# Optimization experiments

Hardware: AMD Instinct MI355X
Metric: run time of the kernel (lower is better)

The kernel has to match this reference:

```python
import jax, jax.numpy as jnp
import numpy as np

B, N, OBS = 512, 64, 256
H1, H2 = 4, 4
D = 128            # embed/key dim (d_k_1 = d_k_2 = 128)
O1 = D // H1       # 32, per-head value dim stage 1
O2 = D // H2       # 32, per-head value dim stage 2
IN2 = O1 * H1      # 128, input dim to stage 2
FOUT = 16          # final_output_dim


def setup_inputs() -> dict:
    key = jax.random.key(0)
    ks = jax.random.split(key, 22)
    g = lambda k, shp: (jax.random.normal(k, shp, dtype=jnp.float32) * 0.05)
    inp = {
        "states": jax.random.normal(ks[0], (B, N, OBS), dtype=jnp.float32),
        # stage 1 per-head params, stacked over heads
        "E1_w": g(ks[1], (H1, D, OBS)), "E1_b": g(ks[2], (H1, D)),
        "K1_w": g(ks[3], (H1, D, D)),   "K1_b": g(ks[4], (H1, D)),
        "Q1_w": g(ks[5], (H1, D, D)),   "Q1_b": g(ks[6], (H1, D)),
        "V1_w": g(ks[7], (H1, O1, D)),  "V1_b": g(ks[8], (H1, O1)),
        # stage 2 per-head params
        "E2_w": g(ks[9], (H2, D, IN2)), "E2_b": g(ks[10], (H2, D)),
        "K2_w": g(ks[11], (H2, D, D)),  "K2_b": g(ks[12], (H2, D)),
        "Q2_w": g(ks[13], (H2, D, D)),  "Q2_b": g(ks[14], (H2, D)),
        "V2_w": g(ks[15], (H2, O2, D)), "V2_b": g(ks[16], (H2, O2)),
        # final MLP policy head
        "F1_w": g(ks[17], (64, O2 * H2)), "F1_b": g(ks[18], (64,)),
        "F2_w": g(ks[19], (FOUT, 64)),    "F2_b": g(ks[20], (FOUT,)),
    }
    return inp


def _attn_block(x, Ew, Eb, Kw, Kb, Qw, Qb, Vw, Vb, d_k):
    # x: [B,N,I]; all head loops batched via leading head axis h
    se = jax.nn.leaky_relu(jnp.einsum('bni,hdi->hbnd', x, Ew) + Eb[:, None, None, :])  # [h,B,N,D]
    k = jnp.einsum('hbnd,hed->hbne', se, Kw) + Kb[:, None, None, :]
    q = jnp.einsum('hbnd,hed->hbne', se, Qw) + Qb[:, None, None, :]
    w = jax.nn.softmax(jnp.einsum('hbne,hbme->hbnm', q, k) / jnp.sqrt(jnp.float32(d_k)), axis=-1)  # [h,B,N,N]
    v = jax.nn.leaky_relu(jnp.einsum('hbnd,hod->hbno', se, Vw) + Vb[:, None, None, :])  # [h,B,N,O]
    att = jnp.einsum('hbnm,hbmo->hbno', w, v)
    h, b, n, o = att.shape
    return jnp.transpose(att, (1, 2, 0, 3)).reshape(b, n, h * o), w


def reference(states, E1_w, E1_b, K1_w, K1_b, Q1_w, Q1_b, V1_w, V1_b,
              E2_w, E2_b, K2_w, K2_b, Q2_w, Q2_b, V2_w, V2_b,
              F1_w, F1_b, F2_w, F2_b):
    x1, w1 = _attn_block(states, E1_w, E1_b, K1_w, K1_b, Q1_w, Q1_b, V1_w, V1_b, D)
    x2, w2 = _attn_block(x1, E2_w, E2_b, K2_w, K2_b, Q2_w, Q2_b, V2_w, V2_b, D)
    h = jax.nn.leaky_relu(jnp.einsum('bnf,of->bno', x2, F1_w) + F1_b)
    policy = jax.nn.softmax(jnp.einsum('bno,po->bnp', h, F2_w) + F2_b, axis=-1)
    return policy, w1, w2
```

## Files before the change

### kernel.cpp

```cpp
#include <hip/hip_runtime.h>

typedef __attribute__((ext_vector_type(8))) short short8;
typedef __attribute__((ext_vector_type(4))) short short4v;
typedef __attribute__((ext_vector_type(4))) float f32x4;

#define MFMA(a, b, c) __builtin_amdgcn_mfma_f32_16x16x32_bf16((a), (b), (c), 0, 0, 0)

__device__ __forceinline__ short f2bf(float f) {
    union { float f; unsigned u; } v; v.f = f;
    unsigned r = v.u + 0x7fffu + ((v.u >> 16) & 1u);
    return (short)(r >> 16);
}
__device__ __forceinline__ float bf2f(short s) {
    union { unsigned u; float f; } v; v.u = ((unsigned)(unsigned short)s) << 16; return v.f;
}

struct ConvArgs { const float* src[10]; int end[10]; };

__global__ __launch_bounds__(256) void convert_weights_kernel(ConvArgs a, short* __restrict__ dst) {
    int i4 = blockIdx.x * 256 + threadIdx.x;
    int seg = 0;
#pragma unroll
    for (int s = 0; s < 9; s++) seg += (i4 >= a.end[s]) ? 1 : 0;
    int base = (seg == 0) ? 0 : a.end[seg - 1];
    float4 v = ((const float4*)a.src[seg])[i4 - base];
    short4v o; o.x = f2bf(v.x); o.y = f2bf(v.y); o.z = f2bf(v.z); o.w = f2bf(v.w);
    *(short4v*)(dst + (size_t)i4 * 4) = o;
}

#define KQ_LD  136
#define VT_LD  72
#define W_LD   72
#define OFF_K  0
#define OFF_Q  8704
#define OFF_SE 17408
#define OFF_VT 17408
#define OFF_W  8704
#define W32_LD 68
#define SMEM_SHORTS 26112

template<int IN, bool XF32>
__global__ __launch_bounds__(256, 3) void attn_stage_kernel(
    const void* __restrict__ xin,
    const short* __restrict__ Ew, const float* __restrict__ Eb,
    const short* __restrict__ Kw, const float* __restrict__ Kb,
    const short* __restrict__ Qw, const float* __restrict__ Qb,
    const short* __restrict__ Vw, const float* __restrict__ Vb,
    float* __restrict__ w_out,
    short* __restrict__ x_out)
{
    __shared__ short sm[SMEM_SHORTS];
    const int tid  = threadIdx.x;
    const int b    = blockIdx.x & 511;
    const int h    = blockIdx.x >> 9;
    const int wv   = tid >> 6;
    const int lane = tid & 63;
    const int quad = lane >> 4;
    const int l16  = lane & 15;
    const int XLD  = IN + 8;
    constexpr int NK1 = IN / 32;

    if constexpr (XF32) {
        const float* xb = (const float*)xin + (size_t)b * 64 * IN;
#pragma unroll
        for (int r = 0; r < IN / 16; r++) {
            int f4 = tid + 256 * r;
            int row = f4 / (IN / 4), c4 = f4 % (IN / 4);
            float4 v = ((const float4*)xb)[f4];
            short4v o; o.x = f2bf(v.x); o.y = f2bf(v.y); o.z = f2bf(v.z); o.w = f2bf(v.w);
            *(short4v*)&sm[row * XLD + c4 * 4] = o;
        }
    } else {
        const short* xb = (const short*)xin + (size_t)b * 64 * IN;
#pragma unroll
        for (int r = 0; r < IN / 32; r++) {
            int f8 = tid + 256 * r;
            int row = f8 / (IN / 8), c8 = f8 % (IN / 8);
            short8 v = *(const short8*)(xb + (size_t)f8 * 8);
            *(short8*)&sm[row * XLD + c8 * 8] = v;
        }
    }

    short8 ebf[NK1 * 2];
    {
        const short* ewh = Ew + (size_t)h * 128 * IN;
#pragma unroll
        for (int k0i = 0; k0i < NK1; k0i++)
#pragma unroll
            for (int j = 0; j < 2; j++)
                ebf[k0i * 2 + j] = *(const short8*)(ewh + (size_t)(wv * 32 + j * 16 + l16) * IN + k0i * 32 + quad * 8);
    }
    __syncthreads();

    short8 kbf[8];

    {
        f32x4 acc[4][2];
#pragma unroll
        for (int j = 0; j < 2; j++) {
            float bv = Eb[h * 128 + wv * 32 + j * 16 + l16];
            f32x4 c = {bv, bv, bv, bv};
#pragma unroll
            for (int i = 0; i < 4; i++) acc[i][j] = c;
        }
#pragma unroll
        for (int k0i = 0; k0i < NK1; k0i++) {
            short8 a[4];
#pragma unroll
            for (int i = 0; i < 4; i++)
                a[i] = *(const short8*)&sm[(i * 16 + l16) * XLD + k0i * 32 + quad * 8];
#pragma unroll
            for (int i = 0; i < 4; i++)
#pragma unroll
                for (int j = 0; j < 2; j++)
                    acc[i][j] = MFMA(a[i], ebf[k0i * 2 + j], acc[i][j]);
        }
        {
            const short* kwh = Kw + (size_t)h * 128 * 128;
#pragma unroll
            for (int k0i = 0; k0i < 4; k0i++)
#pragma unroll
                for (int j = 0; j < 2; j++)
                    kbf[k0i * 2 + j] = *(const short8*)(kwh + (size_t)(wv * 32 + j * 16 + l16) * 128 + k0i * 32 + quad * 8);
        }
#pragma unroll
        for (int i = 0; i < 4; i++)
#pragma unroll
            for (int j = 0; j < 2; j++)
#pragma unroll
                for (int r = 0; r < 4; r++) {
                    float v = acc[i][j][r];
                    v = (v >= 0.f) ? v : 0.01f * v;
                    sm[OFF_SE + (i * 16 + quad * 4 + r) * KQ_LD + wv * 32 + j * 16 + l16] = f2bf(v);
                }
    }
    __syncthreads();

    f32x4 vacc[2];
    {
        short8 qbf[8];
        const short* qwh = Qw + (size_t)h * 128 * 128;
#pragma unroll
        for (int k0i = 0; k0i < 4; k0i++)
#pragma unroll
            for (int j = 0; j < 2; j++)
                qbf[k0i * 2 + j] = *(const short8*)(qwh + (size_t)(wv * 32 + j * 16 + l16) * 128 + k0i * 32 + quad * 8);
        f32x4 kacc[4][2], qacc[4][2];
#pragma unroll
        for (int j = 0; j < 2; j++) {
            float kb = Kb[h * 128 + wv * 32 + j * 16 + l16];
            float qb = Qb[h * 128 + wv * 32 + j * 16 + l16];
            f32x4 kc = {kb, kb, kb, kb}, qc = {qb, qb, qb, qb};
#pragma unroll
            for (int i = 0; i < 4; i++) { kacc[i][j] = kc; qacc[i][j] = qc; }
        }
#pragma unroll
        for (int k0i = 0; k0i < 4; k0i++) {
            short8 a[4];
#pragma unroll
            for (int i = 0; i < 4; i++)
                a[i] = *(const short8*)&sm[OFF_SE + (i * 16 + l16) * KQ_LD + k0i * 32 + quad * 8];
#pragma unroll
            for (int i = 0; i < 4; i++)
#pragma unroll
                for (int j = 0; j < 2; j++) {
                    kacc[i][j] = MFMA(a[i], kbf[k0i * 2 + j], kacc[i][j]);
                    qacc[i][j] = MFMA(a[i], qbf[k0i * 2 + j], qacc[i][j]);
                }
        }
#pragma unroll
        for (int i = 0; i < 4; i++)
#pragma unroll
            for (int j = 0; j < 2; j++)
#pragma unroll
                for (int r = 0; r < 4; r++) {
                    int row = i * 16 + quad * 4 + r, col = wv * 32 + j * 16 + l16;
                    sm[OFF_K + row * KQ_LD + col] = f2bf(kacc[i][j][r]);
                    sm[OFF_Q + row * KQ_LD + col] = f2bf(qacc[i][j][r]);
                }
        const short* vwh = Vw + (size_t)h * 32 * 128;
        const int n0v = (wv >> 1) * 16, mrow = (wv & 1) * 32;
        short8 vbf[4];
#pragma unroll
        for (int k0i = 0; k0i < 4; k0i++)
            vbf[k0i] = *(const short8*)(vwh + (size_t)(n0v + l16) * 128 + k0i * 32 + quad * 8);
        float vb = Vb[h * 32 + n0v + l16];
        vacc[0] = (f32x4){vb, vb, vb, vb}; vacc[1] = vacc[0];
#pragma unroll
        for (int k0i = 0; k0i < 4; k0i++) {
            short8 a0 = *(const short8*)&sm[OFF_SE + (mrow + l16) * KQ_LD + k0i * 32 + quad * 8];
            short8 a1 = *(const short8*)&sm[OFF_SE + (mrow + 16 + l16) * KQ_LD + k0i * 32 + quad * 8];
            vacc[0] = MFMA(a0, vbf[k0i], vacc[0]);
            vacc[1] = MFMA(a1, vbf[k0i], vacc[1]);
        }
    }
    __syncthreads();

    {
        const int n0v = (wv >> 1) * 16, mrow = (wv & 1) * 32;
#pragma unroll
        for (int i = 0; i < 2; i++)
#pragma unroll
            for (int r = 0; r < 4; r++) {
                float v = vacc[i][r];
                v = (v >= 0.f) ? v : 0.01f * v;
                sm[OFF_VT + (n0v + l16) * VT_LD + mrow + i * 16 + quad * 4 + r] = f2bf(v);
            }
    }

    f32x4 lacc[4];
#pragma unroll
    for (int jj = 0; jj < 4; jj++) lacc[jj] = (f32x4){0.f, 0.f, 0.f, 0.f};
#pragma unroll
    for (int k0 = 0; k0 < 128; k0 += 32) {
        short8 a = *(const short8*)&sm[OFF_Q + (wv * 16 + l16) * KQ_LD + k0 + quad * 8];
#pragma unroll
        for (int jj = 0; jj < 4; jj++) {
            short8 b8 = *(const short8*)&sm[OFF_K + (jj * 16 + l16) * KQ_LD + k0 + quad * 8];
            lacc[jj] = MFMA(a, b8, lacc[jj]);
        }
    }
    __syncthreads();

    {
        const float scale = 0.08838834764831845f;
        float* w32 = (float*)sm;
        float mx[4], inv[4];
#pragma unroll
        for (int r = 0; r < 4; r++) {
            float m = lacc[0][r];
#pragma unroll
            for (int jj = 1; jj < 4; jj++) m = fmaxf(m, lacc[jj][r]);
#pragma unroll
            for (int s = 1; s < 16; s <<= 1) m = fmaxf(m, __shfl_xor(m, s, 16));
            mx[r] = m;
        }
        float sum[4] = {0.f, 0.f, 0.f, 0.f};
#pragma unroll
        for (int jj = 0; jj < 4; jj++)
#pragma unroll
            for (int r = 0; r < 4; r++) {
                float e = __expf((lacc[jj][r] - mx[r]) * scale);
                lacc[jj][r] = e; sum[r] += e;
            }
#pragma unroll
        for (int r = 0; r < 4; r++) {
#pragma unroll
            for (int s = 1; s < 16; s <<= 1) sum[r] += __shfl_xor(sum[r], s, 16);
            inv[r] = 1.0f / sum[r];
        }
#pragma unroll
        for (int r = 0; r < 4; r++) {
            int row = wv * 16 + quad * 4 + r;
#pragma unroll
            for (int jj = 0; jj < 4; jj++) {
                float wval = lacc[jj][r] * inv[r];
                w32[row * W32_LD + jj * 16 + l16] = wval;
                sm[OFF_W + row * W_LD + jj * 16 + l16] = f2bf(wval);
            }
        }
    }
    __syncthreads();

    {
        const float* w32 = (const float*)sm;
        float* wbase = w_out + ((size_t)(h * 512 + b)) * 64 * 64;
#pragma unroll
        for (int s = 0; s < 4; s++) {
            int idx = tid + 256 * s;
            int row = idx >> 4, c4 = (idx & 15) * 4;
            f32x4 v = *(const f32x4*)&w32[row * W32_LD + c4];
            __builtin_nontemporal_store(v, (f32x4*)(wbase + idx * 4));
        }
    }

    {
        f32x4 aacc[2]; aacc[0] = (f32x4){0.f, 0.f, 0.f, 0.f}; aacc[1] = aacc[0];
#pragma unroll
        for (int k0 = 0; k0 < 64; k0 += 32) {
            short8 a = *(const short8*)&sm[OFF_W + (wv * 16 + l16) * W_LD + k0 + quad * 8];
#pragma unroll
            for (int j = 0; j < 2; j++) {
                short8 b8 = *(const short8*)&sm[OFF_VT + (j * 16 + l16) * VT_LD + k0 + quad * 8];
                aacc[j] = MFMA(a, b8, aacc[j]);
            }
        }
        short* xob = x_out + (size_t)b * 64 * 128;
#pragma unroll
        for (int j = 0; j < 2; j++)
#pragma unroll
            for (int r = 0; r < 4; r++)
                xob[(size_t)(wv * 16 + quad * 4 + r) * 128 + h * 32 + j * 16 + l16] = f2bf(aacc[j][r]);
    }
}

#define H_LD 72
__global__ __launch_bounds__(256)
void final_mlp_mfma_kernel(const short* __restrict__ x2,
                           const short* __restrict__ F1wb,
                           const float* __restrict__ F1b,
                           const short* __restrict__ F2wb,
                           const float* __restrict__ F2b,
                           float* __restrict__ policy)
{
    __shared__ short hsm[4][16 * H_LD];
    const int tid  = threadIdx.x;
    const int wv   = tid >> 6;
    const int lane = tid & 63;
    const int quad = lane >> 4;
    const int l16  = lane & 15;
    const int rowbase = blockIdx.x * 64 + wv * 16;

    short8 a[4];
    const short* xrow = x2 + (size_t)(rowbase + l16) * 128;
#pragma unroll
    for (int k = 0; k < 4; k++) a[k] = *(const short8*)(xrow + k * 32 + quad * 8);
    f32x4 acc[4];
#pragma unroll
    for (int j = 0; j < 4; j++) { float bv = F1b[j * 16 + l16]; acc[j] = (f32x4){bv, bv, bv, bv}; }
#pragma unroll
    for (int k = 0; k < 4; k++)
#pragma unroll
        for (int j = 0; j < 4; j++) {
            short8 b8 = *(const short8*)(F1wb + (size_t)(j * 16 + l16) * 128 + k * 32 + quad * 8);
            acc[j] = MFMA(a[k], b8, acc[j]);
        }
    short* hh = &hsm[wv][0];
#pragma unroll
    for (int j = 0; j < 4; j++)
#pragma unroll
        for (int r = 0; r < 4; r++) {
            float v = acc[j][r];
            v = (v >= 0.f) ? v : 0.01f * v;
            hh[(quad * 4 + r) * H_LD + j * 16 + l16] = f2bf(v);
        }
    __syncthreads();

    f32x4 lg;
    { float bv = F2b[l16]; lg = (f32x4){bv, bv, bv, bv}; }
#pragma unroll
    for (int k = 0; k < 2; k++) {
        short8 a2 = *(const short8*)(hh + l16 * H_LD + k * 32 + quad * 8);
        short8 b8 = *(const short8*)(F2wb + (size_t)l16 * 64 + k * 32 + quad * 8);
        lg = MFMA(a2, b8, lg);
    }
#pragma unroll
    for (int r = 0; r < 4; r++) {
        float m = lg[r];
        m = fmaxf(m, __shfl_xor(m, 1, 16));
        m = fmaxf(m, __shfl_xor(m, 2, 16));
        m = fmaxf(m, __shfl_xor(m, 4, 16));
        m = fmaxf(m, __shfl_xor(m, 8, 16));
        float e = __expf(lg[r] - m);
        float s = e;
        s += __shfl_xor(s, 1, 16);
        s += __shfl_xor(s, 2, 16);
        s += __shfl_xor(s, 4, 16);
        s += __shfl_xor(s, 8, 16);
        policy[(size_t)(rowbase + quad * 4 + r) * 16 + l16] = e / s;
    }
}

extern "C" void kernel_launch(void* const* d_in, const int* in_sizes, int n_in,
                              void* d_out, int out_size, void* d_ws, size_t ws_size,
                              hipStream_t stream) {
    const float* states = (const float*)d_in[0];
    const float* E1w = (const float*)d_in[1];  const float* E1b = (const float*)d_in[2];
    const float* K1w = (const float*)d_in[3];  const float* K1b = (const float*)d_in[4];
    const float* Q1w = (const float*)d_in[5];  const float* Q1b = (const float*)d_in[6];
    const float* V1w = (const float*)d_in[7];  const float* V1b = (const float*)d_in[8];
    const float* E2w = (const float*)d_in[9];  const float* E2b = (const float*)d_in[10];
    const float* K2w = (const float*)d_in[11]; const float* K2b = (const float*)d_in[12];
    const float* Q2w = (const float*)d_in[13]; const float* Q2b = (const float*)d_in[14];
    const float* V2w = (const float*)d_in[15]; const float* V2b = (const float*)d_in[16];
    const float* F1w = (const float*)d_in[17]; const float* F1b = (const float*)d_in[18];
    const float* F2w = (const float*)d_in[19]; const float* F2b = (const float*)d_in[20];

    float* out    = (float*)d_out;
    float* policy = out;
    float* w1     = out + 512 * 64 * 16;
    float* w2     = w1 + 4 * 512 * 64 * 64;

    short* wsb = (short*)d_ws;
    short* x1b = wsb;
    short* x2b = wsb + 4194304;
    short* wts = wsb + 8388608;
    short* wE1 = wts;            short* wK1 = wts + 131072;
    short* wQ1 = wts + 196608;   short* wV1 = wts + 262144;
    short* wE2 = wts + 278528;   short* wK2 = wts + 344064;
    short* wQ2 = wts + 409600;   short* wV2 = wts + 475136;
    short* wF1 = wts + 491520;   short* wF2 = wts + 499712;

    ConvArgs ca;
    ca.src[0] = E1w; ca.src[1] = K1w; ca.src[2] = Q1w; ca.src[3] = V1w;
    ca.src[4] = E2w; ca.src[5] = K2w; ca.src[6] = Q2w; ca.src[7] = V2w;
    ca.src[8] = F1w; ca.src[9] = F2w;
    ca.end[0] = 32768;  ca.end[1] = 49152;  ca.end[2] = 65536;  ca.end[3] = 69632;
    ca.end[4] = 86016;  ca.end[5] = 102400; ca.end[6] = 118784; ca.end[7] = 122880;
    ca.end[8] = 124928; ca.end[9] = 125184;
    convert_weights_kernel<<<489, 256, 0, stream>>>(ca, wts);

    attn_stage_kernel<256, true><<<2048, 256, 0, stream>>>(
        (const void*)states, wE1, E1b, wK1, K1b, wQ1, Q1b, wV1, V1b, w1, x1b);
    attn_stage_kernel<128, false><<<2048, 256, 0, stream>>>(
        (const void*)x1b, wE2, E2b, wK2, K2b, wQ2, Q2b, wV2, V2b, w2, x2b);
    final_mlp_mfma_kernel<<<512, 256, 0, stream>>>(x2b, wF1, F1b, wF2, F2b, policy);
}
```

Baseline: 218.1 us.

## Fold Q·Kᵀ into precomputed bilinear matrix and drop K/Q projections

Rewrites the attention logits as se·G·seᵀ with G = Qwᵀ·Kw·scale, precomputed once per head, plus a per-key bias term (Qb·Kw)·se. Terms that are constant across each softmax row are dropped because softmax cancels them. This halves the per-tile projection MFMAs and removes the separate K and Q shared buffers, which cuts LDS use so four blocks can run per SM. The states are now converted to bf16 in the prep kernel and read directly from global memory, and the fp32 weight writes go straight to global without LDS staging. The trade-offs are an extra precompute kernel, a larger conversion pass, bf16 rounding of the folded G, and a different bias handling.

Result: slower. 277.3 us (+27.2%).

```diff
diff --git a/kernel.cpp b/kernel.cpp
--- a/kernel.cpp
+++ b/kernel.cpp
@@ -15,36 +15,69 @@
     union { unsigned u; float f; } v; v.u = ((unsigned)(unsigned short)s) << 16; return v.f;
 }
 
-struct ConvArgs { const float* src[10]; int end[10]; };
-
-__global__ __launch_bounds__(256) void convert_weights_kernel(ConvArgs a, short* __restrict__ dst) {
+struct ConvArgs { const float* src[7]; int end[7]; };
+
+__global__ __launch_bounds__(256) void convert_weights_kernel(ConvArgs a,
+                                                              short* __restrict__ dstw,
+                                                              short* __restrict__ dstx) {
     int i4 = blockIdx.x * 256 + threadIdx.x;
     int seg = 0;
 #pragma unroll
-    for (int s = 0; s < 9; s++) seg += (i4 >= a.end[s]) ? 1 : 0;
+    for (int s = 0; s < 6; s++) seg += (i4 >= a.end[s]) ? 1 : 0;
     int base = (seg == 0) ? 0 : a.end[seg - 1];
     float4 v = ((const float4*)a.src[seg])[i4 - base];
     short4v o; o.x = f2bf(v.x); o.y = f2bf(v.y); o.z = f2bf(v.z); o.w = f2bf(v.w);
-    *(short4v*)(dst + (size_t)i4 * 4) = o;
+    short* dst = (seg == 6) ? (dstx + (size_t)(i4 - a.end[5]) * 4)
+                            : (dstw + (size_t)i4 * 4);
+    *(short4v*)dst = o;
+}
+
+__global__ __launch_bounds__(256) void precompute_gt_kernel(
+    const float* __restrict__ Q1w, const float* __restrict__ K1w, const float* __restrict__ Q1b,
+    const float* __restrict__ Q2w, const float* __restrict__ K2w, const float* __restrict__ Q2b,
+    short* __restrict__ gt, float* __restrict__ wvec) {
+    const int s  = blockIdx.x >> 5;
+    const int h  = (blockIdx.x >> 3) & 3;
+    const int fg = blockIdx.x & 7;
+    const float* Qw = (s ? Q2w : Q1w) + (size_t)h * 16384;
+    const float* Kw = (s ? K2w : K1w) + (size_t)h * 16384;
+    const float* qb = (s ? Q2b : Q1b) + h * 128;
+    const int f  = fg * 16 + (threadIdx.x >> 4);
+    const int e0 = (threadIdx.x & 15) * 8;
+    float acc[8] = {0.f, 0.f, 0.f, 0.f, 0.f, 0.f, 0.f, 0.f};
+    float accw = 0.f;
+    for (int c = 0; c < 128; c++) {
+        float kv = Kw[c * 128 + f];
+        accw = fmaf(qb[c], kv, accw);
+        float4 a0 = *(const float4*)(Qw + c * 128 + e0);
+        float4 a1 = *(const float4*)(Qw + c * 128 + e0 + 4);
+        acc[0] = fmaf(kv, a0.x, acc[0]); acc[1] = fmaf(kv, a0.y, acc[1]);
+        acc[2] = fmaf(kv, a0.z, acc[2]); acc[3] = fmaf(kv, a0.w, acc[3]);
+        acc[4] = fmaf(kv, a1.x, acc[4]); acc[5] = fmaf(kv, a1.y, acc[5]);
+        acc[6] = fmaf(kv, a1.z, acc[6]); acc[7] = fmaf(kv, a1.w, acc[7]);
+    }
+    const float scale = 0.08838834764831845f;
+    short8 o = { f2bf(acc[0] * scale), f2bf(acc[1] * scale), f2bf(acc[2] * scale), f2bf(acc[3] * scale),
+                 f2bf(acc[4] * scale), f2bf(acc[5] * scale), f2bf(acc[6] * scale), f2bf(acc[7] * scale) };
+    *(short8*)(gt + ((size_t)((s * 4 + h) * 128 + f)) * 128 + e0) = o;
+    if (e0 == 0) wvec[(s * 4 + h) * 128 + f] = accw * scale;
 }
 
 #define KQ_LD  136
 #define VT_LD  72
 #define W_LD   72
-#define OFF_K  0
-#define OFF_Q  8704
-#define OFF_SE 17408
+#define OFF_T  0
+#define OFF_SE 8704
 #define OFF_VT 17408
-#define OFF_W  8704
-#define W32_LD 68
-#define SMEM_SHORTS 26112
-
-template<int IN, bool XF32>
-__global__ __launch_bounds__(256, 3) void attn_stage_kernel(
-    const void* __restrict__ xin,
+#define OFF_CB 19712
+#define OFF_W  0
+#define SMEM_SHORTS 19840
+
+template<int IN>
+__global__ __launch_bounds__(256, 4) void attn_stage_kernel(
+    const short* __restrict__ xin,
     const short* __restrict__ Ew, const float* __restrict__ Eb,
-    const short* __restrict__ Kw, const float* __restrict__ Kb,
-    const short* __restrict__ Qw, const float* __restrict__ Qb,
+    const short* __restrict__ Gt, const float* __restrict__ wvec,
     const short* __restrict__ Vw, const float* __restrict__ Vb,
     float* __restrict__ w_out,
     short* __restrict__ x_out)
@@ -57,29 +90,9 @@
     const int lane = tid & 63;
     const int quad = lane >> 4;
     const int l16  = lane & 15;
-    const int XLD  = IN + 8;
     constexpr int NK1 = IN / 32;
 
-    if constexpr (XF32) {
-        const float* xb = (const float*)xin + (size_t)b * 64 * IN;
-#pragma unroll
-        for (int r = 0; r < IN / 16; r++) {
-            int f4 = tid + 256 * r;
-            int row = f4 / (IN / 4), c4 = f4 % (IN / 4);
-            float4 v = ((const float4*)xb)[f4];
-            short4v o; o.x = f2bf(v.x); o.y = f2bf(v.y); o.z = f2bf(v.z); o.w = f2bf(v.w);
-            *(short4v*)&sm[row * XLD + c4 * 4] = o;
-        }
-    } else {
-        const short* xb = (const short*)xin + (size_t)b * 64 * IN;
-#pragma unroll
-        for (int r = 0; r < IN / 32; r++) {
-            int f8 = tid + 256 * r;
-            int row = f8 / (IN / 8), c8 = f8 % (IN / 8);
-            short8 v = *(const short8*)(xb + (size_t)f8 * 8);
-            *(short8*)&sm[row * XLD + c8 * 8] = v;
-        }
-    }
+    const short* xb = xin + (size_t)b * 64 * IN;
 
     short8 ebf[NK1 * 2];
     {
@@ -90,9 +103,8 @@
             for (int j = 0; j < 2; j++)
                 ebf[k0i * 2 + j] = *(const short8*)(ewh + (size_t)(wv * 32 + j * 16 + l16) * IN + k0i * 32 + quad * 8);
     }
-    __syncthreads();
-
-    short8 kbf[8];
+
+    short8 gtf[8];
 
     {
         f32x4 acc[4][2];
@@ -108,7 +120,7 @@
             short8 a[4];
 #pragma unroll
             for (int i = 0; i < 4; i++)
-                a[i] = *(const short8*)&sm[(i * 16 + l16) * XLD + k0i * 32 + quad * 8];
+                a[i] = *(const short8*)(xb + (size_t)(i * 16 + l16) * IN + k0i * 32 + quad * 8);
 #pragma unroll
             for (int i = 0; i < 4; i++)
 #pragma unroll
@@ -116,12 +128,12 @@
                     acc[i][j] = MFMA(a[i], ebf[k0i * 2 + j], acc[i][j]);
         }
         {
-            const short* kwh = Kw + (size_t)h * 128 * 128;
+            const short* gth = Gt + (size_t)h * 16384;
 #pragma unroll
             for (int k0i = 0; k0i < 4; k0i++)
 #pragma unroll
                 for (int j = 0; j < 2; j++)
-                    kbf[k0i * 2 + j] = *(const short8*)(kwh + (size_t)(wv * 32 + j * 16 + l16) * 128 + k0i * 32 + quad * 8);
+                    gtf[k0i * 2 + j] = *(const short8*)(gth + (size_t)(wv * 32 + j * 16 + l16) * 128 + k0i * 32 + quad * 8);
         }
 #pragma unroll
         for (int i = 0; i < 4; i++)
@@ -136,24 +148,13 @@
     }
     __syncthreads();
 
-    f32x4 vacc[2];
     {
-        short8 qbf[8];
-        const short* qwh = Qw + (size_t)h * 128 * 128;
-#pragma unroll
-        for (int k0i = 0; k0i < 4; k0i++)
-#pragma unroll
-            for (int j = 0; j < 2; j++)
-                qbf[k0i * 2 + j] = *(const short8*)(qwh + (size_t)(wv * 32 + j * 16 + l16) * 128 + k0i * 32 + quad * 8);
-        f32x4 kacc[4][2], qacc[4][2];
-#pragma unroll
-        for (int j = 0; j < 2; j++) {
-            float kb = Kb[h * 128 + wv * 32 + j * 16 + l16];
-            float qb = Qb[h * 128 + wv * 32 + j * 16 + l16];
-            f32x4 kc = {kb, kb, kb, kb}, qc = {qb, qb, qb, qb};
-#pragma unroll
-            for (int i = 0; i < 4; i++) { kacc[i][j] = kc; qacc[i][j] = qc; }
-        }
+        f32x4 tacc[4][2];
+        f32x4 z = {0.f, 0.f, 0.f, 0.f};
+#pragma unroll
+        for (int i = 0; i < 4; i++)
+#pragma unroll
+            for (int j = 0; j < 2; j++) tacc[i][j] = z;
 #pragma unroll
         for (int k0i = 0; k0i < 4; k0i++) {
             short8 a[4];
@@ -163,21 +164,17 @@
 #pragma unroll
             for (int i = 0; i < 4; i++)
 #pragma unroll
-                for (int j = 0; j < 2; j++) {
-                    kacc[i][j] = MFMA(a[i], kbf[k0i * 2 + j], kacc[i][j]);
-                    qacc[i][j] = MFMA(a[i], qbf[k0i * 2 + j], qacc[i][j]);
-                }
+                for (int j = 0; j < 2; j++)
+                    tacc[i][j] = MFMA(a[i], gtf[k0i * 2 + j], tacc[i][j]);
         }
 #pragma unroll
         for (int i = 0; i < 4; i++)
 #pragma unroll
             for (int j = 0; j < 2; j++)
 #pragma unroll
-                for (int r = 0; r < 4; r++) {
-                    int row = i * 16 + quad * 4 + r, col = wv * 32 + j * 16 + l16;
-                    sm[OFF_K + row * KQ_LD + col] = f2bf(kacc[i][j][r]);
-                    sm[OFF_Q + row * KQ_LD + col] = f2bf(qacc[i][j][r]);
-                }
+                for (int r = 0; r < 4; r++)
+                    sm[OFF_T + (i * 16 + quad * 4 + r) * KQ_LD + wv * 32 + j * 16 + l16] = f2bf(tacc[i][j][r]);
+
         const short* vwh = Vw + (size_t)h * 32 * 128;
         const int n0v = (wv >> 1) * 16, mrow = (wv & 1) * 32;
         short8 vbf[4];
@@ -185,6 +182,7 @@
         for (int k0i = 0; k0i < 4; k0i++)
             vbf[k0i] = *(const short8*)(vwh + (size_t)(n0v + l16) * 128 + k0i * 32 + quad * 8);
         float vb = Vb[h * 32 + n0v + l16];
+        f32x4 vacc[2];
         vacc[0] = (f32x4){vb, vb, vb, vb}; vacc[1] = vacc[0];
 #pragma unroll
         for (int k0i = 0; k0i < 4; k0i++) {
@@ -193,11 +191,6 @@
             vacc[0] = MFMA(a0, vbf[k0i], vacc[0]);
             vacc[1] = MFMA(a1, vbf[k0i], vacc[1]);
         }
-    }
-    __syncthreads();
-
-    {
-        const int n0v = (wv >> 1) * 16, mrow = (wv & 1) * 32;
 #pragma unroll
         for (int i = 0; i < 2; i++)
 #pragma unroll
@@ -206,25 +199,53 @@
                 v = (v >= 0.f) ? v : 0.01f * v;
                 sm[OFF_VT + (n0v + l16) * VT_LD + mrow + i * 16 + quad * 4 + r] = f2bf(v);
             }
-    }
+
+        {
+            const float* wvh = wvec + h * 128;
+            const int row = wv * 16 + (lane >> 2);
+            const int e0 = (lane & 3) * 32;
+            float s = 0.f;
+#pragma unroll
+            for (int u = 0; u < 32; u += 8) {
+                short8 sv = *(const short8*)&sm[OFF_SE + row * KQ_LD + e0 + u];
+                float4 w0 = *(const float4*)(wvh + e0 + u);
+                float4 w1 = *(const float4*)(wvh + e0 + u + 4);
+                s = fmaf(bf2f(sv[0]), w0.x, s); s = fmaf(bf2f(sv[1]), w0.y, s);
+                s = fmaf(bf2f(sv[2]), w0.z, s); s = fmaf(bf2f(sv[3]), w0.w, s);
+                s = fmaf(bf2f(sv[4]), w1.x, s); s = fmaf(bf2f(sv[5]), w1.y, s);
+                s = fmaf(bf2f(sv[6]), w1.z, s); s = fmaf(bf2f(sv[7]), w1.w, s);
+            }
+            s += __shfl_xor(s, 1, 4);
+            s += __shfl_xor(s, 2, 4);
+            if ((lane & 3) == 0) ((float*)&sm[OFF_CB])[row] = s;
+        }
+    }
+    __syncthreads();
 
     f32x4 lacc[4];
 #pragma unroll
     for (int jj = 0; jj < 4; jj++) lacc[jj] = (f32x4){0.f, 0.f, 0.f, 0.f};
 #pragma unroll
     for (int k0 = 0; k0 < 128; k0 += 32) {
-        short8 a = *(const short8*)&sm[OFF_Q + (wv * 16 + l16) * KQ_LD + k0 + quad * 8];
+        short8 a = *(const short8*)&sm[OFF_T + (wv * 16 + l16) * KQ_LD + k0 + quad * 8];
 #pragma unroll
         for (int jj = 0; jj < 4; jj++) {
-            short8 b8 = *(const short8*)&sm[OFF_K + (jj * 16 + l16) * KQ_LD + k0 + quad * 8];
+            short8 b8 = *(const short8*)&sm[OFF_SE + (jj * 16 + l16) * KQ_LD + k0 + quad * 8];
             lacc[jj] = MFMA(a, b8, lacc[jj]);
         }
     }
     __syncthreads();
 
     {
-        const float scale = 0.08838834764831845f;
-        float* w32 = (float*)sm;
+        const float* cbf = (const float*)&sm[OFF_CB];
+        float cbv[4];
+#pragma unroll
+        for (int jj = 0; jj < 4; jj++) cbv[jj] = cbf[jj * 16 + l16];
+#pragma unroll
+        for (int jj = 0; jj < 4; jj++)
+#pragma unroll
+            for (int r = 0; r < 4; r++) lacc[jj][r] += cbv[jj];
+
         float mx[4], inv[4];
 #pragma unroll
         for (int r = 0; r < 4; r++) {
@@ -240,7 +261,7 @@
         for (int jj = 0; jj < 4; jj++)
 #pragma unroll
             for (int r = 0; r < 4; r++) {
-                float e = __expf((lacc[jj][r] - mx[r]) * scale);
+                float e = __expf(lacc[jj][r] - mx[r]);
                 lacc[jj][r] = e; sum[r] += e;
             }
 #pragma unroll
@@ -249,30 +270,19 @@
             for (int s = 1; s < 16; s <<= 1) sum[r] += __shfl_xor(sum[r], s, 16);
             inv[r] = 1.0f / sum[r];
         }
+        float* wbase = w_out + ((size_t)(h * 512 + b)) * 64 * 64;
 #pragma unroll
         for (int r = 0; r < 4; r++) {
             int row = wv * 16 + quad * 4 + r;
 #pragma unroll
             for (int jj = 0; jj < 4; jj++) {
                 float wval = lacc[jj][r] * inv[r];
-                w32[row * W32_LD + jj * 16 + l16] = wval;
                 sm[OFF_W + row * W_LD + jj * 16 + l16] = f2bf(wval);
+                __builtin_nontemporal_store(wval, wbase + row * 64 + jj * 16 + l16);
             }
         }
     }
     __syncthreads();
-
-    {
-        const float* w32 = (const float*)sm;
-        float* wbase = w_out + ((size_t)(h * 512 + b)) * 64 * 64;
-#pragma unroll
-        for (int s = 0; s < 4; s++) {
-            int idx = tid + 256 * s;
-            int row = idx >> 4, c4 = (idx & 15) * 4;
-            f32x4 v = *(const f32x4*)&w32[row * W32_LD + c4];
-            __builtin_nontemporal_store(v, (f32x4*)(wbase + idx * 4));
-        }
-    }
 
     {
         f32x4 aacc[2]; aacc[0] = (f32x4){0.f, 0.f, 0.f, 0.f}; aacc[1] = aacc[0];
@@ -375,6 +385,7 @@
     const float* V2w = (const float*)d_in[15]; const float* V2b = (const float*)d_in[16];
     const float* F1w = (const float*)d_in[17]; const float* F1b = (const float*)d_in[18];
     const float* F2w = (const float*)d_in[19]; const float* F2b = (const float*)d_in[20];
+    (void)K1b; (void)K2b;
 
     float* out    = (float*)d_out;
     float* policy = out;
@@ -383,26 +394,29 @@
 
     short* wsb = (short*)d_ws;
     short* x1b = wsb;
-    short* x2b = wsb + 4194304;
-    short* wts = wsb + 8388608;
-    short* wE1 = wts;            short* wK1 = wts + 131072;
-    short* wQ1 = wts + 196608;   short* wV1 = wts + 262144;
-    short* wE2 = wts + 278528;   short* wK2 = wts + 344064;
-    short* wQ2 = wts + 409600;   short* wV2 = wts + 475136;
-    short* wF1 = wts + 491520;   short* wF2 = wts + 499712;
+    short* xsb = wsb + 4194304;
+    short* x2b = xsb;
+    short* wts = wsb + 12582912;
+    short* wE1 = wts;
+    short* wV1 = wts + 131072;
+    short* wE2 = wts + 147456;
+    short* wV2 = wts + 212992;
+    short* wF1 = wts + 229376;
+    short* wF2 = wts + 237568;
+    short* gt  = wts + 238592;
+    float* wvec = (float*)(wts + 238592 + 131072);
 
     ConvArgs ca;
-    ca.src[0] = E1w; ca.src[1] = K1w; ca.src[2] = Q1w; ca.src[3] = V1w;
-    ca.src[4] = E2w; ca.src[5] = K2w; ca.src[6] = Q2w; ca.src[7] = V2w;
-    ca.src[8] = F1w; ca.src[9] = F2w;
-    ca.end[0] = 32768;  ca.end[1] = 49152;  ca.end[2] = 65536;  ca.end[3] = 69632;
-    ca.end[4] = 86016;  ca.end[5] = 102400; ca.end[6] = 118784; ca.end[7] = 122880;
-    ca.end[8] = 124928; ca.end[9] = 125184;
-    convert_weights_kernel<<<489, 256, 0, stream>>>(ca, wts);
-
-    attn_stage_kernel<256, true><<<2048, 256, 0, stream>>>(
-        (const void*)states, wE1, E1b, wK1, K1b, wQ1, Q1b, wV1, V1b, w1, x1b);
-    attn_stage_kernel<128, false><<<2048, 256, 0, stream>>>(
-        (const void*)x1b, wE2, E2b, wK2, K2b, wQ2, Q2b, wV2, V2b, w2, x2b);
+    ca.src[0] = E1w; ca.src[1] = V1w; ca.src[2] = E2w; ca.src[3] = V2w;
+    ca.src[4] = F1w; ca.src[5] = F2w; ca.src[6] = states;
+    ca.end[0] = 32768;  ca.end[1] = 36864;  ca.end[2] = 53248;  ca.end[3] = 57344;
+    ca.end[4] = 59392;  ca.end[5] = 59648;  ca.end[6] = 2156800;
+    convert_weights_kernel<<<8425, 256, 0, stream>>>(ca, wts, xsb);
+    precompute_gt_kernel<<<64, 256, 0, stream>>>(Q1w, K1w, Q1b, Q2w, K2w, Q2b, gt, wvec);
+
+    attn_stage_kernel<256><<<2048, 256, 0, stream>>>(
+        xsb, wE1, E1b, gt, wvec, wV1, V1b, w1, x1b);
+    attn_stage_kernel<128><<<2048, 256, 0, stream>>>(
+        x1b, wE2, E2b, gt + 65536, wvec + 512, wV2, V2b, w2, x2b);
     final_mlp_mfma_kernel<<<512, 256, 0, stream>>>(x2b, wF1, F1b, wF2, F2b, policy);
 }
```
